# Kernel tuning notes

Measured on AMD Instinct MI355X. Metric: run time of the kernel, lower is better.

## Reference

```python
import math
import jax, jax.numpy as jnp
import numpy as np

N_HEADS = 16
THETA = 10000.0


def _rope_cos_sin(S, head_dim):
    half = head_dim // 2
    inv_freq = 1.0 / (THETA ** (jnp.arange(half, dtype=jnp.float32) / half))
    t = jnp.arange(S, dtype=jnp.float32)
    freqs = t[:, None] * inv_freq[None, :]  # [S, half]
    return jnp.cos(freqs), jnp.sin(freqs)


def _apply_rope(x, cos, sin):
    # x: [B, H, S, D] float32; cos/sin: [S, D//2]
    half = x.shape[-1] // 2
    x1, x2 = x[..., :half], x[..., half:]
    c = cos[None, None, :, :]
    s = sin[None, None, :, :]
    return jnp.concatenate([x1 * c - x2 * s, x1 * s + x2 * c], axis=-1)


def setup_inputs() -> dict:
    key = jax.random.key(0)
    k1, k2, k3 = jax.random.split(key, 3)
    B, S, D = 4, 2048, 1024
    x = jax.random.normal(k1, (B, S, D), dtype=jnp.float32)
    w_qkv = jax.random.normal(k2, (3 * D, D), dtype=jnp.float32) * (1.0 / math.sqrt(D))
    w_out = jax.random.normal(k3, (D, D), dtype=jnp.float32) * (1.0 / math.sqrt(D))
    return {"x": x, "w_qkv": w_qkv, "w_out": w_out}


def reference(x, w_qkv, w_out):
    B, S, D = x.shape
    H = N_HEADS
    hd = D // H

    qkv = x @ w_qkv.T  # [B, S, 3D]
    q, k, v = jnp.split(qkv, 3, axis=-1)

    def reshape(t):
        return t.reshape(B, S, H, hd).transpose(0, 2, 1, 3)  # [B,H,S,hd]

    q, k, v = reshape(q), reshape(k), reshape(v)

    cos, sin = _rope_cos_sin(S, hd)
    q = _apply_rope(q.astype(jnp.float32), cos, sin).astype(x.dtype)
    k = _apply_rope(k.astype(jnp.float32), cos, sin).astype(x.dtype)

    scale = math.sqrt(hd)
    scores = jnp.einsum("bhsd,bhtd->bhst", q, k) / scale  # [B,H,S,S]
    causal = jnp.tril(jnp.ones((S, S), dtype=bool))
    scores = jnp.where(causal[None, None], scores, -jnp.inf)
    attn = jax.nn.softmax(scores.astype(jnp.float32), axis=-1).astype(x.dtype)

    out = jnp.einsum("bhst,bhtd->bhsd", attn, v)  # [B,H,S,hd]
    out = out.transpose(0, 2, 1, 3).reshape(B, S, D)
    return out @ w_out.T
```

## Files before the change

### kernel.cpp

```cpp
#include <hip/hip_runtime.h>
#include <hip/hip_bf16.h>

#define DEV static __device__ __forceinline__

typedef unsigned short u16;
typedef unsigned int u32;
typedef __attribute__((ext_vector_type(8))) short short8;
typedef __attribute__((ext_vector_type(4))) float f32x4;
typedef __attribute__((ext_vector_type(16))) float f32x16;
typedef __attribute__((ext_vector_type(4))) u32 u32x4;

static constexpr int Bsz = 4, Ssz = 2048, Dsz = 1024, Hn = 16, HD = 64;
static constexpr int Mrows = Bsz * Ssz;

DEV u16 f2bu(float f) {
  union { float f; u32 u; } a; a.f = f;
  u32 u = a.u;
  u32 r = (u + 0x7FFFu + ((u >> 16) & 1u)) >> 16;
  return (u16)r;
}
DEV float b2f(u16 v) {
  union { u32 u; float f; } a; a.u = ((u32)v) << 16;
  return a.f;
}
DEV u32 pk2(float lo, float hi2) {
  __hip_bfloat162 t = __float22bfloat162_rn(make_float2(lo, hi2));
  u32 r; __builtin_memcpy(&r, &t, 4); return r;
}
DEV f32x16 mfma3232(short8 a, short8 b, f32x16 c) {
  return __builtin_amdgcn_mfma_f32_32x32x16_bf16(a, b, c, 0, 0, 0);
}
DEV float max3f(float a, float b, float c) { return fmaxf(fmaxf(a, b), c); }
DEV float ex2(float x) { return __builtin_amdgcn_exp2f(x); }

__global__ void k_cast(const float4* __restrict__ in, ushort4* __restrict__ out, int n4) {
  int stride = gridDim.x * blockDim.x;
  for (int i = blockIdx.x * blockDim.x + threadIdx.x; i < n4; i += stride) {
    float4 v = in[i];
    ushort4 o;
    o.x = f2bu(v.x); o.y = f2bu(v.y); o.z = f2bu(v.z); o.w = f2bu(v.w);
    out[i] = o;
  }
}

__global__ void k_ropetab(float2* __restrict__ cst) {
  int i = blockIdx.x * blockDim.x + threadIdx.x;
  if (i >= Ssz * 32) return;
  int s = i >> 5, d = i & 31;
  float inv = powf(10000.0f, -(float)d / 32.0f);
  float fr = (float)s * inv;
  cst[i] = make_float2(cosf(fr), sinf(fr));
}

__global__ __launch_bounds__(256) void k_vtrans(const u16* __restrict__ qkv,
                                                u16* __restrict__ vt) {
  __shared__ u16 tile[64][68];
  const int t = threadIdx.x;
  const int bh = blockIdx.y;
  const int b = bh >> 4, h = bh & 15;
  const int s0 = blockIdx.x * 64;
#pragma unroll
  for (int it = 0; it < 4; ++it) {
    int idx = it * 256 + t;
    int d4 = (idx & 15) * 4;
    int sl = idx >> 4;
    ushort4 v = *(const ushort4*)(qkv + ((size_t)(b * Ssz + s0 + sl)) * 3072 + 2048 + h * 64 + d4);
    *(ushort4*)&tile[sl][d4] = v;
  }
  __syncthreads();
#pragma unroll
  for (int it = 0; it < 4; ++it) {
    int idx = it * 256 + t;
    int sl4 = (idx & 15) * 4;
    int d = idx >> 4;
    ushort4 o;
    o.x = tile[sl4 + 0][d];
    o.y = tile[sl4 + 1][d];
    o.z = tile[sl4 + 2][d];
    o.w = tile[sl4 + 3][d];
    *(ushort4*)(vt + ((size_t)(bh * 64 + d)) * Ssz + s0 + sl4) = o;
  }
}

DEV void cp16(const u16* g, u16* l) {
  __builtin_amdgcn_global_load_lds((const __attribute__((address_space(1))) u32*)g,
                                   (__attribute__((address_space(3))) u32*)l, 16, 0, 0);
}

template <bool OUTBF16>
__global__ __launch_bounds__(256) void k_gemm(const u16* __restrict__ A,
                                              const u16* __restrict__ W,
                                              void* __restrict__ C, int N, int K,
                                              const float2* __restrict__ cst, int cpx) {
  __shared__ __align__(16) u16 Asm[2][128 * 32];
  __shared__ __align__(16) u16 Bsm[2][128 * 32];
  const int tid = threadIdx.x;
  const int wid = tid >> 6, lane = tid & 63;
  const int lr = lane & 15, u = lane >> 4;
  const int wm = wid >> 1, wn = wid & 1;

  const int wg = blockIdx.x;
  const int xcd = wg & 7;
  const int j = wg >> 3;
  const int brow = (j / cpx) * 128;
  const int bcol = (xcd * cpx + j % cpx) * 128;

  const int srow = lane >> 2;
  const int soct = ((lane & 3) ^ (srow & 3)) * 8;
  const u16* aS0 = A + (size_t)(brow + wid * 32 + srow) * K + soct;
  const u16* aS1 = aS0 + (size_t)16 * K;
  const u16* bS0 = W + (size_t)(bcol + wid * 32 + srow) * K + soct;
  const u16* bS1 = bS0 + (size_t)16 * K;
  const int dOff = wid * 1024;

  const int aRow = wm * 64 + lr;
  const int bRow = wn * 64 + lr;
  const int rslot = (u ^ (lr & 3)) * 8;

  f32x4 acc[4][4];
#pragma unroll
  for (int i = 0; i < 4; ++i)
#pragma unroll
    for (int j2 = 0; j2 < 4; ++j2) acc[i][j2] = (f32x4){0.f, 0.f, 0.f, 0.f};

  const int nt = K >> 5;
  cp16(aS0, Asm[0] + dOff);
  cp16(aS1, Asm[0] + dOff + 512);
  cp16(bS0, Bsm[0] + dOff);
  cp16(bS1, Bsm[0] + dOff + 512);

  for (int t = 0; t < nt; ++t) {
    __syncthreads();
    if (t + 1 < nt) {
      const int nb = (t + 1) & 1;
      const int kn = (t + 1) << 5;
      cp16(aS0 + kn, Asm[nb] + dOff);
      cp16(aS1 + kn, Asm[nb] + dOff + 512);
      cp16(bS0 + kn, Bsm[nb] + dOff);
      cp16(bS1 + kn, Bsm[nb] + dOff + 512);
    }
    const u16* ab = Asm[t & 1];
    const u16* bb = Bsm[t & 1];
    short8 af[4], bfr[4];
#pragma unroll
    for (int mr = 0; mr < 4; ++mr) af[mr] = *(const short8*)(ab + (aRow + mr * 16) * 32 + rslot);
#pragma unroll
    for (int nr = 0; nr < 4; ++nr) bfr[nr] = *(const short8*)(bb + (bRow + nr * 16) * 32 + rslot);
#pragma unroll
    for (int mr = 0; mr < 4; ++mr)
#pragma unroll
      for (int nr = 0; nr < 4; ++nr)
        acc[mr][nr] =
            __builtin_amdgcn_mfma_f32_16x16x32_bf16(af[mr], bfr[nr], acc[mr][nr], 0, 0, 0);
  }

  const int row0 = brow + wm * 64 + u * 4;
  const int col0 = bcol + wn * 64 + lr;
  if (OUTBF16) {
    const int rmode = (bcol < 1024) ? 0 : (bcol < 2048) ? 1 : 2;
    const float sc = (rmode == 0) ? 0.18033688f : 1.0f;
#pragma unroll
    for (int mr = 0; mr < 4; ++mr)
#pragma unroll
      for (int r = 0; r < 4; ++r) {
        const int row = row0 + mr * 16 + r;
        size_t base = (size_t)row * N + col0;
        u16* cp = (u16*)C + base;
        if (rmode < 2) {
          const int s = row & 2047;
          const float2 c0 = cst[s * 32 + lr];
          const float2 c1 = cst[s * 32 + 16 + lr];
          const float x10 = acc[mr][0][r], x11 = acc[mr][1][r];
          const float x20 = acc[mr][2][r], x21 = acc[mr][3][r];
          cp[0]  = f2bu((x10 * c0.x - x20 * c0.y) * sc);
          cp[16] = f2bu((x11 * c1.x - x21 * c1.y) * sc);
          cp[32] = f2bu((x10 * c0.y + x20 * c0.x) * sc);
          cp[48] = f2bu((x11 * c1.y + x21 * c1.x) * sc);
        } else {
#pragma unroll
          for (int nr = 0; nr < 4; ++nr) cp[nr * 16] = f2bu(acc[mr][nr][r]);
        }
      }
  } else {
#pragma unroll
    for (int mr = 0; mr < 4; ++mr)
#pragma unroll
      for (int r = 0; r < 4; ++r) {
        size_t base = (size_t)(row0 + mr * 16 + r) * N + col0;
#pragma unroll
        for (int nr = 0; nr < 4; ++nr) ((float*)C)[base + nr * 16] = acc[mr][nr][r];
      }
  }
}

__global__ __launch_bounds__(256, 4) void k_attn(const u16* __restrict__ qkv,
                                                 const u16* __restrict__ vt,
                                                 u16* __restrict__ obuf) {
  __shared__ __align__(16) u16 Ksm[2][64 * 64];
  __shared__ __align__(16) u16 Vsm[2][64 * 64];

  const int tid = threadIdx.x;
  const int wid = tid >> 6;
  const int lane = tid & 63;
  const int l31 = lane & 31;
  const int hi = lane >> 5;
  const int r7 = l31 & 7;

  const int fid = blockIdx.x;
  const int a = fid & 3, bq = (fid >> 8) & 3;
  const int bh = (fid >> 2) & 63;
  const int sel = a ^ bq;
  const int qt = (sel == 0) ? bq : (sel == 1) ? 7 - bq : (sel == 2) ? 8 + bq : 15 - bq;

  const int b = bh >> 4;
  const int h = bh & 15;

  const float NEG = -__builtin_inff();

  const int srow = lane >> 3;
  const int scol = ((lane & 7) ^ srow) * 8;
  const u16* ksrc0 = qkv + (size_t)(b * Ssz + wid * 16 + srow) * 3072 + 1024 + h * 64 + scol;
  const u16* ksrc1 = ksrc0 + (size_t)8 * 3072;
  const u16* vsrc0 = vt + ((size_t)bh * 64 + wid * 16 + srow) * Ssz + scol;
  const u16* vsrc1 = vsrc0 + (size_t)8 * Ssz;
  u16* kD0 = Ksm[0] + wid * 1024;
  u16* vD0 = Vsm[0] + wid * 1024;

  const int q0 = qt * 128;
  const int qrow = q0 + (wid << 5) + l31;

  const u16* qptr = qkv + (size_t)(b * Ssz + qrow) * 3072 + h * 64 + hi * 8;
  short8 qf[4];
#pragma unroll
  for (int s = 0; s < 4; ++s) qf[s] = *(const short8*)(qptr + s * 16);

  f32x16 o0 = {0.f}, o1 = {0.f};
  float m = NEG, lsum = 0.f;

  const int ntiles = 2 * qt + 2;
  const int lastT = 2 * qt + (wid >> 1);

  cp16(ksrc0, kD0);
  cp16(ksrc1, kD0 + 512);
  cp16(vsrc0, vD0);
  cp16(vsrc1, vD0 + 512);

  const u16* kS0 = ksrc0 + (size_t)64 * 3072;
  const u16* kS1 = ksrc1 + (size_t)64 * 3072;
  const u16* vS0 = vsrc0 + 64;
  const u16* vS1 = vsrc1 + 64;

  for (int t = 0; t < ntiles; ++t) {
    __syncthreads();
    if (t + 1 < ntiles) {
      const int nb = (t + 1) & 1;
      cp16(kS0, kD0 + nb * 4096);
      cp16(kS1, kD0 + nb * 4096 + 512);
      cp16(vS0, vD0 + nb * 4096);
      cp16(vS1, vD0 + nb * 4096 + 512);
      kS0 += (size_t)64 * 3072;
      kS1 += (size_t)64 * 3072;
      vS0 += 64;
      vS1 += 64;
    }
    if (t > lastT) continue;

    const u16* kbuf = Ksm[t & 1];
    const u16* vbuf = Vsm[t & 1];
    const int kv0 = t << 6;

    f32x16 st0 = {0.f}, st1 = {0.f};
    __builtin_amdgcn_s_setprio(1);
#pragma unroll
    for (int s = 0; s < 4; ++s) {
      const int slot = (((2 * s + hi) ^ r7) << 3);
      short8 k0 = *(const short8*)(kbuf + l31 * 64 + slot);
      short8 k1 = *(const short8*)(kbuf + (32 + l31) * 64 + slot);
      st0 = mfma3232(k0, qf[s], st0);
      st1 = mfma3232(k1, qf[s], st1);
    }
    __builtin_amdgcn_s_setprio(0);

    if (t == lastT) {
      const int kb0 = kv0 + 4 * hi;
#pragma unroll
      for (int r = 0; r < 16; ++r) {
        const int ko = (r & 3) + 8 * (r >> 2);
        if (kb0 + ko > qrow) st0[r] = NEG;
        if (kb0 + 32 + ko > qrow) st1[r] = NEG;
      }
    }

    float c0 = max3f(st0[0], st0[1], st0[2]);
    c0 = max3f(c0, st0[3], st1[0]);
    c0 = max3f(c0, st1[1], st1[2]);
    c0 = fmaxf(c0, st1[3]);
    float c1 = max3f(st0[4], st0[5], st0[6]);
    c1 = max3f(c1, st0[7], st1[4]);
    c1 = max3f(c1, st1[5], st1[6]);
    c1 = fmaxf(c1, st1[7]);
    float c2 = max3f(st0[8], st0[9], st0[10]);
    c2 = max3f(c2, st0[11], st1[8]);
    c2 = max3f(c2, st1[9], st1[10]);
    c2 = fmaxf(c2, st1[11]);
    float c3 = max3f(st0[12], st0[13], st0[14]);
    c3 = max3f(c3, st0[15], st1[12]);
    c3 = max3f(c3, st1[13], st1[14]);
    c3 = fmaxf(c3, st1[15]);
    float pm = fmaxf(max3f(c0, c1, c2), c3);
    pm = fmaxf(pm, __shfl_xor(pm, 32));

    if (!__all(pm <= m + 8.0f)) {
      const float mn = fmaxf(m, pm);
      const float corr = ex2(m - mn);
      lsum *= corr;
      o0 *= corr;
      o1 *= corr;
      m = mn;
    }

    float rsp[4] = {0.f, 0.f, 0.f, 0.f};
#pragma unroll
    for (int r = 0; r < 16; ++r) {
      const float p0 = ex2(st0[r] - m);
      const float p1 = ex2(st1[r] - m);
      st0[r] = p0;
      st1[r] = p1;
      rsp[r & 3] += p0 + p1;
    }
    float rs = (rsp[0] + rsp[1]) + (rsp[2] + rsp[3]);
    rs += __shfl_xor(rs, 32);
    lsum += rs;

    u32 wa[8], wb[8];
#pragma unroll
    for (int g = 0; g < 4; ++g) {
      wa[g] = pk2(st0[4 * g + 0], st0[4 * g + 1]);
      wb[g] = pk2(st0[4 * g + 2], st0[4 * g + 3]);
      wa[4 + g] = pk2(st1[4 * g + 0], st1[4 * g + 1]);
      wb[4 + g] = pk2(st1[4 * g + 2], st1[4 * g + 3]);
    }

#pragma unroll
    for (int s = 0; s < 4; ++s) {
      const u32 uA0 = wa[2 * s], uA1 = wa[2 * s + 1];
      const u32 uB0 = wb[2 * s], uB1 = wb[2 * s + 1];
      const u32 tA0 = __shfl_xor(uA0, 32), tA1 = __shfl_xor(uA1, 32);
      const u32 tB0 = __shfl_xor(uB0, 32), tB1 = __shfl_xor(uB1, 32);
      u32x4 pw;
      pw.x = hi ? tA1 : uA0;
      pw.y = hi ? tB1 : uB0;
      pw.z = hi ? uA1 : tA0;
      pw.w = hi ? uB1 : tB0;
      short8 pfrag = *(short8*)&pw;
      const int slot = (((2 * s + hi) ^ r7) << 3);
      short8 v0 = *(const short8*)(vbuf + l31 * 64 + slot);
      short8 v1 = *(const short8*)(vbuf + (32 + l31) * 64 + slot);
      __builtin_amdgcn_s_setprio(1);
      o0 = mfma3232(v0, pfrag, o0);
      o1 = mfma3232(v1, pfrag, o1);
      __builtin_amdgcn_s_setprio(0);
    }
  }

  const float inv = 1.0f / lsum;
  u16* orow = obuf + (size_t)(b * Ssz + qrow) * 1024 + h * 64;
#pragma unroll
  for (int j = 0; j < 4; ++j) {
    ushort4 s0, s1;
    s0.x = f2bu(o0[4 * j + 0] * inv);
    s0.y = f2bu(o0[4 * j + 1] * inv);
    s0.z = f2bu(o0[4 * j + 2] * inv);
    s0.w = f2bu(o0[4 * j + 3] * inv);
    s1.x = f2bu(o1[4 * j + 0] * inv);
    s1.y = f2bu(o1[4 * j + 1] * inv);
    s1.z = f2bu(o1[4 * j + 2] * inv);
    s1.w = f2bu(o1[4 * j + 3] * inv);
    *(ushort4*)(orow + 8 * j + 4 * hi) = s0;
    *(ushort4*)(orow + 32 + 8 * j + 4 * hi) = s1;
  }
}

extern "C" void kernel_launch(void* const* d_in, const int* in_sizes, int n_in,
                              void* d_out, int out_size, void* d_ws, size_t ws_size,
                              hipStream_t stream) {
  const float* x = (const float*)d_in[0];
  const float* wqkv = (const float*)d_in[1];
  const float* wout = (const float*)d_in[2];

  char* ws = (char*)d_ws;
  u16* xb      = (u16*)(ws + 0);
  u16* wqkvb   = (u16*)(ws + 16777216);
  u16* woutb   = (u16*)(ws + 23068672);
  u16* qkv     = (u16*)(ws + 25165824);
  u16* vt      = (u16*)(ws + 75497472);
  u16* obuf    = (u16*)(ws + 92274688);
  float2* cst  = (float2*)(ws + 109051904);

  k_cast<<<2048, 256, 0, stream>>>((const float4*)x, (ushort4*)xb, Mrows * Dsz / 4);
  k_cast<<<2048, 256, 0, stream>>>((const float4*)wqkv, (ushort4*)wqkvb, 3 * Dsz * Dsz / 4);
  k_cast<<<1024, 256, 0, stream>>>((const float4*)wout, (ushort4*)woutb, Dsz * Dsz / 4);
  k_ropetab<<<256, 256, 0, stream>>>(cst);

  k_gemm<true><<<1536, 256, 0, stream>>>(xb, wqkvb, qkv, 3072, 1024, cst, 3);

  k_vtrans<<<dim3(32, 64), 256, 0, stream>>>(qkv, vt);

  k_attn<<<1024, 256, 0, stream>>>(qkv, vt, obuf);

  k_gemm<false><<<512, 256, 0, stream>>>(obuf, woutb, d_out, 1024, 1024, nullptr, 1);
}
```

Measured before the change: 193.7 us.

## Double GEMM K-tile to 64 with 8-way XOR swizzle and priority hints

```diff
diff --git a/kernel.cpp b/kernel.cpp
--- a/kernel.cpp
+++ b/kernel.cpp
@@ -88,12 +88,12 @@
 }
 
 template <bool OUTBF16>
-__global__ __launch_bounds__(256) void k_gemm(const u16* __restrict__ A,
-                                              const u16* __restrict__ W,
-                                              void* __restrict__ C, int N, int K,
-                                              const float2* __restrict__ cst, int cpx) {
-  __shared__ __align__(16) u16 Asm[2][128 * 32];
-  __shared__ __align__(16) u16 Bsm[2][128 * 32];
+__global__ __launch_bounds__(256, 2) void k_gemm(const u16* __restrict__ A,
+                                                 const u16* __restrict__ W,
+                                                 void* __restrict__ C, int N, int K,
+                                                 const float2* __restrict__ cst, int cpx) {
+  __shared__ __align__(16) u16 Asm[2][128 * 64];
+  __shared__ __align__(16) u16 Bsm[2][128 * 64];
   const int tid = threadIdx.x;
   const int wid = tid >> 6, lane = tid & 63;
   const int lr = lane & 15, u = lane >> 4;
@@ -105,17 +105,16 @@
   const int brow = (j / cpx) * 128;
   const int bcol = (xcd * cpx + j % cpx) * 128;
 
-  const int srow = lane >> 2;
-  const int soct = ((lane & 3) ^ (srow & 3)) * 8;
-  const u16* aS0 = A + (size_t)(brow + wid * 32 + srow) * K + soct;
-  const u16* aS1 = aS0 + (size_t)16 * K;
-  const u16* bS0 = W + (size_t)(bcol + wid * 32 + srow) * K + soct;
-  const u16* bS1 = bS0 + (size_t)16 * K;
-  const int dOff = wid * 1024;
-
-  const int aRow = wm * 64 + lr;
-  const int bRow = wn * 64 + lr;
-  const int rslot = (u ^ (lr & 3)) * 8;
+  const int rw = wid * 32 + (lane >> 3);
+  const int octS = ((lane & 7) ^ (rw & 7)) * 8;
+  const u16* aS = A + (size_t)(brow + rw) * K + octS;
+  const u16* bS = W + (size_t)(bcol + rw) * K + octS;
+  const int dBase = wid * 2048 + lane * 8;
+
+  const int aBase = (wm * 64 + lr) * 64;
+  const int bBase = (wn * 64 + lr) * 64;
+  const int o0 = (u ^ (lane & 7)) * 8;
+  const int o1 = ((4 + u) ^ (lane & 7)) * 8;
 
   f32x4 acc[4][4];
 #pragma unroll
@@ -123,36 +122,55 @@
 #pragma unroll
     for (int j2 = 0; j2 < 4; ++j2) acc[i][j2] = (f32x4){0.f, 0.f, 0.f, 0.f};
 
-  const int nt = K >> 5;
-  cp16(aS0, Asm[0] + dOff);
-  cp16(aS1, Asm[0] + dOff + 512);
-  cp16(bS0, Bsm[0] + dOff);
-  cp16(bS1, Bsm[0] + dOff + 512);
+  const int nt = K >> 6;
+
+#define STG(kk, bb)                                          \
+  do {                                                       \
+    cp16(aS + (kk), Asm[bb] + dBase);                        \
+    cp16(aS + (size_t)8 * K + (kk), Asm[bb] + dBase + 512);  \
+    cp16(aS + (size_t)16 * K + (kk), Asm[bb] + dBase + 1024);\
+    cp16(aS + (size_t)24 * K + (kk), Asm[bb] + dBase + 1536);\
+    cp16(bS + (kk), Bsm[bb] + dBase);                        \
+    cp16(bS + (size_t)8 * K + (kk), Bsm[bb] + dBase + 512);  \
+    cp16(bS + (size_t)16 * K + (kk), Bsm[bb] + dBase + 1024);\
+    cp16(bS + (size_t)24 * K + (kk), Bsm[bb] + dBase + 1536);\
+  } while (0)
+
+  STG(0, 0);
 
   for (int t = 0; t < nt; ++t) {
-    __syncthreads();
-    if (t + 1 < nt) {
-      const int nb = (t + 1) & 1;
-      const int kn = (t + 1) << 5;
-      cp16(aS0 + kn, Asm[nb] + dOff);
-      cp16(aS1 + kn, Asm[nb] + dOff + 512);
-      cp16(bS0 + kn, Bsm[nb] + dOff);
-      cp16(bS1 + kn, Bsm[nb] + dOff + 512);
-    }
+    asm volatile("s_waitcnt vmcnt(0)" ::: "memory");
+    __builtin_amdgcn_s_barrier();
+    if (t + 1 < nt) STG((t + 1) << 6, (t + 1) & 1);
     const u16* ab = Asm[t & 1];
     const u16* bb = Bsm[t & 1];
-    short8 af[4], bfr[4];
-#pragma unroll
-    for (int mr = 0; mr < 4; ++mr) af[mr] = *(const short8*)(ab + (aRow + mr * 16) * 32 + rslot);
-#pragma unroll
-    for (int nr = 0; nr < 4; ++nr) bfr[nr] = *(const short8*)(bb + (bRow + nr * 16) * 32 + rslot);
+    short8 a0[4], a1[4], b0[4], b1[4];
+#pragma unroll
+    for (int mr = 0; mr < 4; ++mr) {
+      a0[mr] = *(const short8*)(ab + aBase + mr * 1024 + o0);
+      a1[mr] = *(const short8*)(ab + aBase + mr * 1024 + o1);
+    }
+#pragma unroll
+    for (int nr = 0; nr < 4; ++nr) {
+      b0[nr] = *(const short8*)(bb + bBase + nr * 1024 + o0);
+      b1[nr] = *(const short8*)(bb + bBase + nr * 1024 + o1);
+    }
+    __builtin_amdgcn_s_setprio(1);
 #pragma unroll
     for (int mr = 0; mr < 4; ++mr)
 #pragma unroll
       for (int nr = 0; nr < 4; ++nr)
         acc[mr][nr] =
-            __builtin_amdgcn_mfma_f32_16x16x32_bf16(af[mr], bfr[nr], acc[mr][nr], 0, 0, 0);
-  }
+            __builtin_amdgcn_mfma_f32_16x16x32_bf16(a0[mr], b0[nr], acc[mr][nr], 0, 0, 0);
+#pragma unroll
+    for (int mr = 0; mr < 4; ++mr)
+#pragma unroll
+      for (int nr = 0; nr < 4; ++nr)
+        acc[mr][nr] =
+            __builtin_amdgcn_mfma_f32_16x16x32_bf16(a1[mr], b1[nr], acc[mr][nr], 0, 0, 0);
+    __builtin_amdgcn_s_setprio(0);
+  }
+#undef STG
 
   const int row0 = brow + wm * 64 + u * 4;
   const int col0 = bcol + wn * 64 + lr;
```

Result: no change. 190.2 us (-1.8%).
